# Performance work log

Hardware: AMD Instinct MI355X
Metric: run time of the kernel (lower is better)

## Reference

```python
import math
import jax, jax.numpy as jnp
import numpy as np


def setup_inputs() -> dict:
    key = jax.random.key(0)
    kq, kk, kv, kb, km = jax.random.split(key, 5)
    B, Q, H, C = 2, 2048, 16, 64
    q = jax.random.normal(kq, (B, Q, H, C), jnp.float32)
    k = jax.random.normal(kk, (B, Q, H, C), jnp.float32)
    v = jax.random.normal(kv, (B, Q, H, C), jnp.float32)
    b = jax.random.normal(kb, (B, H, Q, Q), jnp.float32)
    m = jnp.sort(jax.random.randint(km, (B, Q), 0, 4), axis=-1).astype(jnp.int32)
    return {"q": q, "k": k, "v": v, "b": b, "m": m}


def reference(q, k, v, b, m):
    # q,k,v: (B, S, H, C); b: (B, H, S, S); m: (B, S) segment ids (self-attn)
    sm_scale = 1.0 / math.sqrt(q.shape[-1])
    n_q, n_k = q.shape[1], k.shape[1]
    logits = jnp.einsum('bqhc,bkhc->bhqk', q, k).astype(jnp.float32)
    # segment mask: (B, 1, Q, K), True where query/key share a segment id
    seg_mask = (m[:, :, None] == m[:, None, :])[:, None, :, :]
    causal_mask = jnp.tril(jnp.ones((1, 1, n_q, n_k), dtype=bool))
    mask = jnp.logical_and(seg_mask, causal_mask)
    logits = jnp.where(mask, logits, -jnp.inf)
    weights = jax.nn.softmax(logits * sm_scale + b.astype(jnp.float32), axis=-1).astype(q.dtype)
    out = jnp.einsum('bhqk,bkhc->bqhc', weights, v)
    return out.astype(jnp.float32)
```

## Files before the change

kernel.cpp:

```cpp
#include <hip/hip_runtime.h>
#include <hip/hip_bf16.h>
#include <math.h>

#define NB 2
#define SEQ 2048
#define NH 16
#define HD 64
#define QT 64
#define KT 64

typedef short short8 __attribute__((ext_vector_type(8)));
typedef float f32x4 __attribute__((ext_vector_type(4)));
typedef int i32x4 __attribute__((ext_vector_type(4)));
typedef unsigned int u32;
typedef u32 u32x2 __attribute__((ext_vector_type(2)));
typedef u32 u32x4 __attribute__((ext_vector_type(4)));

__device__ __forceinline__ unsigned short f2bf(float f) {
  union { float f; unsigned u; } x; x.f = f;
  unsigned r = x.u + 0x7fffu + ((x.u >> 16) & 1u);
  return (unsigned short)(r >> 16);
}

__device__ __forceinline__ u32 pkbf(float a, float b) {
  u32 r;
  asm("v_cvt_pk_bf16_f32 %0, %1, %2" : "=v"(r) : "v"(a), "v"(b));
  return r;
}


__global__ __launch_bounds__(256, 3) void attn_fwd(
    const float* __restrict__ Qg, const float* __restrict__ Kg,
    const float* __restrict__ Vg, const float* __restrict__ Bg,
    const int* __restrict__ Mg, float* __restrict__ Og)
{
  const int h = blockIdx.x, qt = blockIdx.y, b = blockIdx.z;
  const int q0 = qt * QT;
  const int tid = threadIdx.x;
  const int wave = tid >> 6, lane = tid & 63;
  const int l16 = lane & 15, lhi = lane >> 4;

  __shared__ __align__(16) unsigned short Ks[KT][72];
  __shared__ __align__(16) unsigned short Vt[HD][72];
  __shared__ __align__(16) unsigned short Ps[4][16][72];

  const int* mb = Mg + b * SEQ;
  const int mqf = mb[q0];
  const int mql = mb[q0 + QT - 1];
  int lo = 0, hi = q0 + 1;
  while (lo < hi) { int mid = (lo + hi) >> 1; if (mb[mid] < mqf) lo = mid + 1; else hi = mid; }
  const int k_lo = lo;
  lo = 0; hi = q0 + QT;
  while (lo < hi) { int mid = (lo + hi) >> 1; if (mb[mid] <= mql) lo = mid + 1; else hi = mid; }
  const int k_hi = lo;

  const int kt0 = k_lo & ~(KT - 1);
  const int nt = (k_hi - kt0 + KT - 1) / KT;

  const int qr = q0 + wave * 16;

  const float* qp = Qg + (((size_t)b * SEQ + qr + l16) * NH + h) * HD;
  short8 qf[2];
  #pragma unroll
  for (int s = 0; s < 2; ++s) {
    f32x4 a0 = *(const f32x4*)(qp + lhi * 8 + 32 * s);
    f32x4 a1 = *(const f32x4*)(qp + lhi * 8 + 32 * s + 4);
    short8 t;
    #pragma unroll
    for (int i = 0; i < 4; ++i) {
      t[i]     = (short)f2bf(a0[i] * 0.125f);
      t[i + 4] = (short)f2bf(a1[i] * 0.125f);
    }
    qf[s] = t;
  }

  int mq[4];
  #pragma unroll
  for (int j = 0; j < 4; ++j) mq[j] = mb[qr + lhi * 4 + j];

  f32x4 oacc[4];
  float rsum[4];
  #pragma unroll
  for (int g = 0; g < 4; ++g) { f32x4 z = {0.f, 0.f, 0.f, 0.f}; oacc[g] = z; }
  #pragma unroll
  for (int j = 0; j < 4; ++j) rsum[j] = 0.f;

  const int krow = tid >> 2, kc0 = (tid & 3) * 16;
  const int kpr  = ((krow & 3) << 4) | (krow >> 2);
  const int tg   = tid >> 4;
  const int vcv  = (tid & 15) * 4;
  const int vr0  = ((tg & 3) << 4) | (tg >> 2);
  const int vc0  = tg * 4;
  const size_t rstride = (size_t)NH * HD;
  const float* kbase = Kg + (((size_t)b * SEQ + krow) * NH + h) * HD + kc0;
  const float* vbase = Vg + (((size_t)b * SEQ + vr0) * NH + h) * HD + vcv;
  const size_t bbase = (((size_t)b * NH + h) * SEQ) * (size_t)SEQ;

  f32x4 kx0, kx1, kx2, kx3, vx0, vx1, vx2, vx3;
  {
    const float* kp = kbase + (size_t)kt0 * rstride;
    kx0 = *(const f32x4*)(kp);      kx1 = *(const f32x4*)(kp + 4);
    kx2 = *(const f32x4*)(kp + 8);  kx3 = *(const f32x4*)(kp + 12);
    const float* vp = vbase + (size_t)kt0 * rstride;
    vx0 = *(const f32x4*)(vp);
    vx1 = *(const f32x4*)(vp + 4 * rstride);
    vx2 = *(const f32x4*)(vp + 8 * rstride);
    vx3 = *(const f32x4*)(vp + 12 * rstride);
  }

  for (int t = 0; t < nt; ++t) {
    const int k0 = kt0 + t * KT;

    const float* bprow = Bg + bbase + (size_t)(qr + lhi * 4) * SEQ + k0 + 4 * l16;
    f32x4 bv4[4];
    #pragma unroll
    for (int j = 0; j < 4; ++j) bv4[j] = *(const f32x4*)(bprow + (size_t)j * SEQ);
    const i32x4 mk = *(const i32x4*)&mb[k0 + 4 * l16];

    __syncthreads();

    {
      u32x4 wa, wb;
      wa[0] = pkbf(kx0[0], kx0[1]); wa[1] = pkbf(kx0[2], kx0[3]);
      wa[2] = pkbf(kx1[0], kx1[1]); wa[3] = pkbf(kx1[2], kx1[3]);
      wb[0] = pkbf(kx2[0], kx2[1]); wb[1] = pkbf(kx2[2], kx2[3]);
      wb[2] = pkbf(kx3[0], kx3[1]); wb[3] = pkbf(kx3[2], kx3[3]);
      *(u32x4*)&Ks[kpr][kc0]     = wa;
      *(u32x4*)&Ks[kpr][kc0 + 8] = wb;
      #pragma unroll
      for (int cc = 0; cc < 4; ++cc) {
        u32x2 wv;
        wv[0] = pkbf(vx0[cc], vx1[cc]);
        wv[1] = pkbf(vx2[cc], vx3[cc]);
        *(u32x2*)&Vt[vcv + cc][vc0] = wv;
      }
    }

    if (t + 1 < nt) {
      const int kn = k0 + KT;
      const float* kp = kbase + (size_t)kn * rstride;
      kx0 = *(const f32x4*)(kp);      kx1 = *(const f32x4*)(kp + 4);
      kx2 = *(const f32x4*)(kp + 8);  kx3 = *(const f32x4*)(kp + 12);
      const float* vp = vbase + (size_t)kn * rstride;
      vx0 = *(const f32x4*)(vp);
      vx1 = *(const f32x4*)(vp + 4 * rstride);
      vx2 = *(const f32x4*)(vp + 8 * rstride);
      vx3 = *(const f32x4*)(vp + 12 * rstride);
    }

    __syncthreads();

    f32x4 sacc[4];
    #pragma unroll
    for (int g = 0; g < 4; ++g) { f32x4 z = {0.f, 0.f, 0.f, 0.f}; sacc[g] = z; }
    #pragma unroll
    for (int s = 0; s < 2; ++s) {
      #pragma unroll
      for (int g = 0; g < 4; ++g) {
        short8 kf = *(const short8*)&Ks[l16 + 16 * g][lhi * 8 + 32 * s];
        sacc[g] = __builtin_amdgcn_mfma_f32_16x16x32_bf16(qf[s], kf, sacc[g], 0, 0, 0);
      }
    }

    const int colk = k0 + 4 * l16;
    #pragma unroll
    for (int g = 0; g < 4; ++g) {
      #pragma unroll
      for (int j = 0; j < 4; ++j) {
        const int rowq = qr + lhi * 4 + j;
        const bool ok = (mk[g] == mq[j]) && (colk + g <= rowq);
        const float s = ok ? (sacc[g][j] + bv4[j][g]) : -50.0f;
        const float p = __expf(s);
        rsum[j] += p;
        Ps[wave][lhi * 4 + j][l16 + 16 * g] = (unsigned short)pkbf(p, p);
      }
    }

    #pragma unroll
    for (int s = 0; s < 2; ++s) {
      short8 pf = *(const short8*)&Ps[wave][l16][lhi * 8 + 32 * s];
      #pragma unroll
      for (int g = 0; g < 4; ++g) {
        short8 vf = *(const short8*)&Vt[l16 + 16 * g][lhi * 8 + 32 * s];
        oacc[g] = __builtin_amdgcn_mfma_f32_16x16x32_bf16(pf, vf, oacc[g], 0, 0, 0);
      }
    }
  }

  #pragma unroll
  for (int j = 0; j < 4; ++j) {
    float r = rsum[j];
    r += __shfl_xor(r, 1); r += __shfl_xor(r, 2);
    r += __shfl_xor(r, 4); r += __shfl_xor(r, 8);
    const float inv = 1.f / r;
    float* op = Og + (((size_t)b * SEQ + qr + lhi * 4 + j) * NH + h) * HD + l16;
    #pragma unroll
    for (int g = 0; g < 4; ++g) op[16 * g] = oacc[g][j] * inv;
  }
}

extern "C" void kernel_launch(void* const* d_in, const int* in_sizes, int n_in,
                              void* d_out, int out_size, void* d_ws, size_t ws_size,
                              hipStream_t stream) {
  const float* q = (const float*)d_in[0];
  const float* k = (const float*)d_in[1];
  const float* v = (const float*)d_in[2];
  const float* bias = (const float*)d_in[3];
  const int* m = (const int*)d_in[4];
  float* out = (float*)d_out;

  dim3 grid(NH, SEQ / QT, NB);
  dim3 block(256);
  hipLaunchKernelGGL(attn_fwd, grid, block, 0, stream, q, k, v, bias, m, out);
}
```

Baseline: 39.11 us.

## Compute transposed QK^T so P feeds PV MFMA from registers, drop LDS staging

Swaps the MFMA operands to compute S^T, so each lane holds probabilities for a single query row across keys. The probabilities are packed straight into bf16 A-operand fragments for the PV MFMA, removing the per-wave Ps shared buffer and its LDS round trip. The K row permutation and V transpose layout are reworked to match, and bias and mask loads now read contiguous runs along each query row. Row sums become one scalar per lane, reduced with cross-lane shuffles at the end.

Result: slower. 43.18 us (+10.4%).

```diff
diff --git a/kernel.cpp b/kernel.cpp
--- a/kernel.cpp
+++ b/kernel.cpp
@@ -42,7 +42,6 @@
 
   __shared__ __align__(16) unsigned short Ks[KT][72];
   __shared__ __align__(16) unsigned short Vt[HD][72];
-  __shared__ __align__(16) unsigned short Ps[4][16][72];
 
   const int* mb = Mg + b * SEQ;
   const int mqf = mb[q0];
@@ -58,8 +57,10 @@
   const int nt = (k_hi - kt0 + KT - 1) / KT;
 
   const int qr = q0 + wave * 16;
-
-  const float* qp = Qg + (((size_t)b * SEQ + qr + l16) * NH + h) * HD;
+  const int qrow = qr + l16;
+  const int mqs = mb[qrow];
+
+  const float* qp = Qg + (((size_t)b * SEQ + qrow) * NH + h) * HD;
   short8 qf[2];
   #pragma unroll
   for (int s = 0; s < 2; ++s) {
@@ -74,27 +75,20 @@
     qf[s] = t;
   }
 
-  int mq[4];
-  #pragma unroll
-  for (int j = 0; j < 4; ++j) mq[j] = mb[qr + lhi * 4 + j];
-
   f32x4 oacc[4];
-  float rsum[4];
+  float rsum = 0.f;
   #pragma unroll
   for (int g = 0; g < 4; ++g) { f32x4 z = {0.f, 0.f, 0.f, 0.f}; oacc[g] = z; }
-  #pragma unroll
-  for (int j = 0; j < 4; ++j) rsum[j] = 0.f;
 
   const int krow = tid >> 2, kc0 = (tid & 3) * 16;
-  const int kpr  = ((krow & 3) << 4) | (krow >> 2);
-  const int tg   = tid >> 4;
-  const int vcv  = (tid & 15) * 4;
-  const int vr0  = ((tg & 3) << 4) | (tg >> 2);
-  const int vc0  = tg * 4;
+  const int kpr  = (krow & 32) | ((krow & 4) << 2) | ((krow & 16) >> 1)
+                 | ((krow & 8) >> 1) | (krow & 3);
+  const int vkb = (tid >> 4) * 4, vcv = (tid & 15) * 4;
   const size_t rstride = (size_t)NH * HD;
   const float* kbase = Kg + (((size_t)b * SEQ + krow) * NH + h) * HD + kc0;
-  const float* vbase = Vg + (((size_t)b * SEQ + vr0) * NH + h) * HD + vcv;
+  const float* vbase = Vg + (((size_t)b * SEQ + vkb) * NH + h) * HD + vcv;
   const size_t bbase = (((size_t)b * NH + h) * SEQ) * (size_t)SEQ;
+  const float* brow = Bg + bbase + (size_t)qrow * SEQ + lhi * 8;
 
   f32x4 kx0, kx1, kx2, kx3, vx0, vx1, vx2, vx3;
   {
@@ -103,19 +97,27 @@
     kx2 = *(const f32x4*)(kp + 8);  kx3 = *(const f32x4*)(kp + 12);
     const float* vp = vbase + (size_t)kt0 * rstride;
     vx0 = *(const f32x4*)(vp);
-    vx1 = *(const f32x4*)(vp + 4 * rstride);
-    vx2 = *(const f32x4*)(vp + 8 * rstride);
-    vx3 = *(const f32x4*)(vp + 12 * rstride);
+    vx1 = *(const f32x4*)(vp + rstride);
+    vx2 = *(const f32x4*)(vp + 2 * rstride);
+    vx3 = *(const f32x4*)(vp + 3 * rstride);
   }
 
   for (int t = 0; t < nt; ++t) {
     const int k0 = kt0 + t * KT;
 
-    const float* bprow = Bg + bbase + (size_t)(qr + lhi * 4) * SEQ + k0 + 4 * l16;
-    f32x4 bv4[4];
-    #pragma unroll
-    for (int j = 0; j < 4; ++j) bv4[j] = *(const f32x4*)(bprow + (size_t)j * SEQ);
-    const i32x4 mk = *(const i32x4*)&mb[k0 + 4 * l16];
+    f32x4 bv[4]; i32x4 mk4[4];
+    {
+      const float* bp = brow + k0;
+      bv[0] = *(const f32x4*)(bp);
+      bv[1] = *(const f32x4*)(bp + 4);
+      bv[2] = *(const f32x4*)(bp + 32);
+      bv[3] = *(const f32x4*)(bp + 36);
+      const int* mp = mb + k0 + lhi * 8;
+      mk4[0] = *(const i32x4*)(mp);
+      mk4[1] = *(const i32x4*)(mp + 4);
+      mk4[2] = *(const i32x4*)(mp + 32);
+      mk4[3] = *(const i32x4*)(mp + 36);
+    }
 
     __syncthreads();
 
@@ -132,7 +134,7 @@
         u32x2 wv;
         wv[0] = pkbf(vx0[cc], vx1[cc]);
         wv[1] = pkbf(vx2[cc], vx3[cc]);
-        *(u32x2*)&Vt[vcv + cc][vc0] = wv;
+        *(u32x2*)&Vt[vcv + cc][vkb] = wv;
       }
     }
 
@@ -143,56 +145,68 @@
       kx2 = *(const f32x4*)(kp + 8);  kx3 = *(const f32x4*)(kp + 12);
       const float* vp = vbase + (size_t)kn * rstride;
       vx0 = *(const f32x4*)(vp);
-      vx1 = *(const f32x4*)(vp + 4 * rstride);
-      vx2 = *(const f32x4*)(vp + 8 * rstride);
-      vx3 = *(const f32x4*)(vp + 12 * rstride);
+      vx1 = *(const f32x4*)(vp + rstride);
+      vx2 = *(const f32x4*)(vp + 2 * rstride);
+      vx3 = *(const f32x4*)(vp + 3 * rstride);
     }
 
     __syncthreads();
 
-    f32x4 sacc[4];
-    #pragma unroll
-    for (int g = 0; g < 4; ++g) { f32x4 z = {0.f, 0.f, 0.f, 0.f}; sacc[g] = z; }
+    f32x4 saccT[4];
+    #pragma unroll
+    for (int g = 0; g < 4; ++g) { f32x4 z = {0.f, 0.f, 0.f, 0.f}; saccT[g] = z; }
     #pragma unroll
     for (int s = 0; s < 2; ++s) {
       #pragma unroll
       for (int g = 0; g < 4; ++g) {
         short8 kf = *(const short8*)&Ks[l16 + 16 * g][lhi * 8 + 32 * s];
-        sacc[g] = __builtin_amdgcn_mfma_f32_16x16x32_bf16(qf[s], kf, sacc[g], 0, 0, 0);
+        saccT[g] = __builtin_amdgcn_mfma_f32_16x16x32_bf16(kf, qf[s], saccT[g], 0, 0, 0);
       }
     }
 
-    const int colk = k0 + 4 * l16;
+    float p[4][4];
     #pragma unroll
     for (int g = 0; g < 4; ++g) {
+      const int kb = k0 + lhi * 8 + (g & 1) * 4 + (g >> 1) * 32;
       #pragma unroll
       for (int j = 0; j < 4; ++j) {
-        const int rowq = qr + lhi * 4 + j;
-        const bool ok = (mk[g] == mq[j]) && (colk + g <= rowq);
-        const float s = ok ? (sacc[g][j] + bv4[j][g]) : -50.0f;
-        const float p = __expf(s);
-        rsum[j] += p;
-        Ps[wave][lhi * 4 + j][l16 + 16 * g] = (unsigned short)pkbf(p, p);
+        const bool ok = (mk4[g][j] == mqs) && (kb + j <= qrow);
+        const float s = ok ? (saccT[g][j] + bv[g][j]) : -50.0f;
+        p[g][j] = __expf(s);
+        rsum += p[g][j];
       }
     }
 
-    #pragma unroll
-    for (int s = 0; s < 2; ++s) {
-      short8 pf = *(const short8*)&Ps[wave][l16][lhi * 8 + 32 * s];
-      #pragma unroll
-      for (int g = 0; g < 4; ++g) {
-        short8 vf = *(const short8*)&Vt[l16 + 16 * g][lhi * 8 + 32 * s];
-        oacc[g] = __builtin_amdgcn_mfma_f32_16x16x32_bf16(pf, vf, oacc[g], 0, 0, 0);
-      }
-    }
-  }
-
+    short8 pf0, pf1;
+    {
+      u32x4 w0, w1;
+      w0[0] = pkbf(p[0][0], p[0][1]); w0[1] = pkbf(p[0][2], p[0][3]);
+      w0[2] = pkbf(p[1][0], p[1][1]); w0[3] = pkbf(p[1][2], p[1][3]);
+      w1[0] = pkbf(p[2][0], p[2][1]); w1[1] = pkbf(p[2][2], p[2][3]);
+      w1[2] = pkbf(p[3][0], p[3][1]); w1[3] = pkbf(p[3][2], p[3][3]);
+      pf0 = *(short8*)&w0;
+      pf1 = *(short8*)&w1;
+    }
+
+    #pragma unroll
+    for (int g = 0; g < 4; ++g) {
+      short8 vf0 = *(const short8*)&Vt[l16 + 16 * g][lhi * 8];
+      oacc[g] = __builtin_amdgcn_mfma_f32_16x16x32_bf16(pf0, vf0, oacc[g], 0, 0, 0);
+    }
+    #pragma unroll
+    for (int g = 0; g < 4; ++g) {
+      short8 vf1 = *(const short8*)&Vt[l16 + 16 * g][lhi * 8 + 32];
+      oacc[g] = __builtin_amdgcn_mfma_f32_16x16x32_bf16(pf1, vf1, oacc[g], 0, 0, 0);
+    }
+  }
+
+  float r = rsum;
+  r += __shfl_xor(r, 16);
+  r += __shfl_xor(r, 32);
   #pragma unroll
   for (int j = 0; j < 4; ++j) {
-    float r = rsum[j];
-    r += __shfl_xor(r, 1); r += __shfl_xor(r, 2);
-    r += __shfl_xor(r, 4); r += __shfl_xor(r, 8);
-    const float inv = 1.f / r;
+    const float rj = __shfl(r, lhi * 4 + j);
+    const float inv = 1.f / rj;
     float* op = Og + (((size_t)b * SEQ + qr + lhi * 4 + j) * NH + h) * HD + l16;
     #pragma unroll
     for (int g = 0; g < 4; ++g) op[16 * g] = oacc[g][j] * inv;
```
